# Performance work log

Measured on AMD Instinct MI355X. Metric: run time of the kernel, lower is better.

## Reference

```python
import jax, jax.numpy as jnp
import numpy as np

NEG_INF = -1e9


def setup_inputs() -> dict:
    key = jax.random.key(0)
    ks = jax.random.split(key, 6)
    B, S, D, H, Dh = 2, 2048, 1024, 16, 64
    scale = 1.0 / np.sqrt(D)
    return {
        "x": jax.random.normal(ks[0], (B, S, D), jnp.float32),
        "W_Q": jax.random.normal(ks[1], (H, D, Dh), jnp.float32) * scale,
        "b_Q": jnp.zeros((H, Dh), jnp.float32),
        "W_K": jax.random.normal(ks[2], (H, D, Dh), jnp.float32) * scale,
        "b_K": jnp.zeros((H, Dh), jnp.float32),
        "W_V": jax.random.normal(ks[3], (H, D, Dh), jnp.float32) * scale,
        "W_O": jax.random.normal(ks[4], (H, Dh, D), jnp.float32) * scale,
        "b_V": jnp.zeros((H, Dh), jnp.float32),
        "b_O": jnp.zeros((H, D), jnp.float32),
    }


def reference(x, W_Q, b_Q, W_K, b_K, W_V, W_O, b_V, b_O):
    # x: [b, s, m]; W_{Q,K,V}: [h, m, d]; W_O: [h, d, m]
    S = x.shape[1]
    d_head = W_Q.shape[-1]

    q = jnp.einsum("bqm,hmd->bqhd", x, W_Q) + b_Q  # [b, q, h, d]
    k = jnp.einsum("bkm,hmd->bkhd", x, W_K) + b_K
    v = jnp.einsum("bkm,hmd->bkhd", x, W_V) + b_V

    scores = jnp.einsum("bqhd,bkhd->bhqk", q, k) / jnp.sqrt(
        jnp.asarray(d_head, x.dtype)
    )  # [b, h, q, k] -- full score matrix, as in the unfused original
    causal = jnp.tril(jnp.ones((S, S), bool))
    scores = jnp.where(causal, scores, jnp.asarray(NEG_INF, x.dtype))
    attn = jax.nn.softmax(scores, axis=-1)

    z = jnp.einsum("bhqk,bkhd->bqhd", attn, v)  # [b, q, h, d]
    # per-head output proj then sum over heads; b_O is [h, m] per the annotation
    out = jnp.einsum("bqhd,hdm->bqm", z, W_O) + jnp.sum(b_O, axis=0)
    return out
```

## Files before the change

### kernel.cpp

```cpp
#include <hip/hip_runtime.h>
#include <cstdint>

typedef unsigned short u16;
typedef short s8v __attribute__((ext_vector_type(8)));
typedef float f4v __attribute__((ext_vector_type(4)));

__device__ __forceinline__ u16 f2b(float f) {
  uint32_t u = __float_as_uint(f);
  u = (u + 0x7FFFu + ((u >> 16) & 1u)) >> 16;
  return (u16)u;
}

__device__ __forceinline__ uint32_t pk2(float a, float b) {
  uint32_t r;
  asm("v_cvt_pk_bf16_f32 %0, %1, %2" : "=v"(r) : "v"(a), "v"(b));
  return r;
}

__device__ __forceinline__ void gload16(const u16* g, u16* l) {
  __builtin_amdgcn_global_load_lds(
      (const __attribute__((address_space(1))) void*)g,
      (__attribute__((address_space(3))) void*)l, 16, 0, 0);
}


__global__ void conv_x(const float* __restrict__ x, u16* __restrict__ xb) {
  int i = blockIdx.x * blockDim.x + threadIdx.x;
  float4 v = ((const float4*)x)[i];
  uint2 o;
  o.x = (uint32_t)f2b(v.x) | ((uint32_t)f2b(v.y) << 16);
  o.y = (uint32_t)f2b(v.z) | ((uint32_t)f2b(v.w) << 16);
  ((uint2*)xb)[i] = o;
}

__global__ void convT_w(const float* __restrict__ W, u16* __restrict__ dst) {
  __shared__ u16 tile[64][65];
  const int m0 = blockIdx.x * 64;
  const int h  = blockIdx.y;
  const int c  = threadIdx.x & 63;
  const int r4 = threadIdx.x >> 6;
  const float* Wh = W + (size_t)h * 65536;
  for (int i = 0; i < 16; ++i) {
    int lm = i * 4 + r4;
    tile[lm][c] = f2b(Wh[(size_t)(m0 + lm) * 64 + c]);
  }
  __syncthreads();
  for (int i = 0; i < 16; ++i) {
    int dd = i * 4 + r4;
    dst[((size_t)h * 64 + dd) * 1024 + m0 + c] = tile[c][dd];
  }
}

__global__ void convT_wo(const float* __restrict__ W, u16* __restrict__ dst) {
  __shared__ u16 tile[64][65];
  const int k0 = blockIdx.x * 64;
  const int m0 = blockIdx.y * 64;
  const int c  = threadIdx.x & 63;
  const int r4 = threadIdx.x >> 6;
  for (int i = 0; i < 16; ++i) {
    int lk = i * 4 + r4;
    tile[lk][c] = f2b(W[(size_t)(k0 + lk) * 1024 + m0 + c]);
  }
  __syncthreads();
  for (int i = 0; i < 16; ++i) {
    int lm = i * 4 + r4;
    dst[(size_t)(m0 + lm) * 1024 + k0 + c] = tile[c][lm];
  }
}

__global__ void convT_v(const u16* __restrict__ QKV, u16* __restrict__ VT) {
  __shared__ u16 tile[64][65];
  const int r0 = blockIdx.x * 64;
  const int c0 = blockIdx.y * 64;
  const int c  = threadIdx.x & 63;
  const int r4 = threadIdx.x >> 6;
  for (int i = 0; i < 16; ++i) {
    int lr = i * 4 + r4;
    tile[lr][c] = QKV[(size_t)(r0 + lr) * 3072 + 2048 + c0 + c];
  }
  __syncthreads();
  for (int i = 0; i < 16; ++i) {
    int lc = i * 4 + r4;
    VT[(size_t)(c0 + lc) * 4096 + r0 + c] = tile[c][lc];
  }
}

__global__ void conv_bias(const float* __restrict__ bQ, const float* __restrict__ bK,
                          const float* __restrict__ bV, const float* __restrict__ bO,
                          float* __restrict__ bqkv, float* __restrict__ bsum) {
  int t = blockIdx.x * 256 + threadIdx.x;
  if (t < 1024)       bqkv[t] = bQ[t];
  else if (t < 2048)  bqkv[t] = bK[t - 1024];
  else if (t < 3072)  bqkv[t] = bV[t - 2048];
  else {
    int m = t - 3072;
    float s = 0.f;
    for (int hh = 0; hh < 16; ++hh) s += bO[hh * 1024 + m];
    bsum[m] = s;
  }
}

template<bool OUT_F32>
__global__ void gemm_bt(const u16* __restrict__ A, const u16* __restrict__ BT,
                        const float* __restrict__ bias, void* __restrict__ Cout,
                        int N, int K, int scale_cols) {
  __shared__ __align__(16) u16 sA[128 * 32];
  __shared__ __align__(16) u16 sB[128 * 32];
  const int tid  = threadIdx.x;
  const int lane = tid & 63, wave = tid >> 6;
  const int wm = wave >> 1, wn = wave & 1;
  const int lq = lane & 15, quad = lane >> 4;
  const int m0 = blockIdx.y * 128, n0 = blockIdx.x * 128;

  f4v acc[4][4] = {};

  for (int k0 = 0; k0 < K; k0 += 32) {
    __syncthreads();
    for (int i = 0; i < 2; ++i) {
      int s = tid + i * 256;
      int row = s >> 2, part = s & 3;
      gload16(A  + (size_t)(m0 + row) * K + k0 + part * 8, &sA[s * 8]);
      gload16(BT + (size_t)(n0 + row) * K + k0 + part * 8, &sB[s * 8]);
    }
    __syncthreads();
    s8v af[4], bfr[4];
    for (int i = 0; i < 4; ++i)
      af[i]  = *(const s8v*)&sA[(wm * 64 + i * 16 + lq) * 32 + quad * 8];
    for (int j = 0; j < 4; ++j)
      bfr[j] = *(const s8v*)&sB[(wn * 64 + j * 16 + lq) * 32 + quad * 8];
    for (int i = 0; i < 4; ++i)
      for (int j = 0; j < 4; ++j)
        acc[i][j] = __builtin_amdgcn_mfma_f32_16x16x32_bf16(af[i], bfr[j], acc[i][j], 0, 0, 0);
  }

  for (int i = 0; i < 4; ++i)
    for (int j = 0; j < 4; ++j) {
      int row = m0 + wm * 64 + i * 16 + quad * 4;
      int col = n0 + wn * 64 + j * 16 + lq;
      float bb = bias[col];
      float sc = (col < scale_cols) ? 0.125f : 1.0f;
      for (int r = 0; r < 4; ++r) {
        float v = (acc[i][j][r] + bb) * sc;
        if (OUT_F32) ((float*)Cout)[(size_t)(row + r) * N + col] = v;
        else         ((u16*)Cout)[(size_t)(row + r) * N + col] = f2b(v);
      }
    }
}

__global__ __launch_bounds__(64, 2) void attn_fwd(const u16* __restrict__ QKV,
                                                  const u16* __restrict__ VT,
                                                  u16* __restrict__ Z) {
  __shared__ __align__(16) u16 sP[2][2][16 * 40];
  const int lane = threadIdx.x;
  const int lq = lane & 15, quad = lane >> 4;

  const int id   = blockIdx.x;
  const int xcd  = id & 7;
  const int slot = id >> 3;
  const int g    = xcd + 8 * (slot >> 6);
  const int s    = slot & 63;
  const int u    = (s < 32) ? (63 - s) : (s - 32);
  const int h = g & 15, b = g >> 4;
  const int qA = u * 32, qB = qA + 16;
  const int nchunk = u + 1;

  const int RS = 3072;
  const u16* base = QKV + (size_t)b * 2048 * RS;
  const u16* Qb  = base + h * 64;
  const u16* Kb  = base + 1024 + h * 64;
  const u16* VTb = VT + (size_t)h * 64 * 4096 + (size_t)b * 2048;

  s8v qfA0 = *(const s8v*)&Qb[(size_t)(qA + lq) * RS + quad * 8];
  s8v qfA1 = *(const s8v*)&Qb[(size_t)(qA + lq) * RS + 32 + quad * 8];
  s8v qfB0 = *(const s8v*)&Qb[(size_t)(qB + lq) * RS + quad * 8];
  s8v qfB1 = *(const s8v*)&Qb[(size_t)(qB + lq) * RS + 32 + quad * 8];

  f4v zA[4] = {}, zB[4] = {};
  float mA = -3.0e38f, lA = 0.f, mB = -3.0e38f, lB = 0.f;

#define LOADK(kf_, c_) do {                                                  \
    const int kk0_ = (c_) * 32;                                              \
    const u16* kr0_ = &Kb[(size_t)(kk0_ + lq) * RS + quad * 8];              \
    const u16* kr1_ = &Kb[(size_t)(kk0_ + 16 + lq) * RS + quad * 8];         \
    kf_[0] = *(const s8v*)kr0_;                                              \
    kf_[1] = *(const s8v*)(kr0_ + 32);                                       \
    kf_[2] = *(const s8v*)kr1_;                                              \
    kf_[3] = *(const s8v*)(kr1_ + 32);                                       \
  } while (0)

#define LOADV(vf_, c_) do {                                                  \
    const int kk0_ = (c_) * 32;                                              \
    vf_[0] = *(const s8v*)&VTb[(size_t)(lq)      * 4096 + kk0_ + quad * 8];  \
    vf_[1] = *(const s8v*)&VTb[(size_t)(16 + lq) * 4096 + kk0_ + quad * 8];  \
    vf_[2] = *(const s8v*)&VTb[(size_t)(32 + lq) * 4096 + kk0_ + quad * 8];  \
    vf_[3] = *(const s8v*)&VTb[(size_t)(48 + lq) * 4096 + kk0_ + quad * 8];  \
  } while (0)

  auto SMW = [&](int c, int qt0, float& mrow, float& lsum, f4v (&zacc)[4],
                 u16* sPt, f4v sacc0, f4v sacc1) {
    float s0[4], s1[4];
    for (int r = 0; r < 4; ++r) { s0[r] = sacc0[r]; s1[r] = sacc1[r]; }
    if (c + 1 == nchunk) {
      const int kb = c * 32;
      for (int r = 0; r < 4; ++r) {
        if (kb + quad * 4 + r > qt0 + lq)      s0[r] = -3.0e38f;
        if (kb + 16 + quad * 4 + r > qt0 + lq) s1[r] = -3.0e38f;
      }
    }
    float lmax = fmaxf(fmaxf(fmaxf(s0[0], s0[1]), fmaxf(s0[2], s0[3])),
                       fmaxf(fmaxf(s1[0], s1[1]), fmaxf(s1[2], s1[3])));
    if (!__all(lmax <= mrow + 8.0f)) {
      float t = lmax;
      t = fmaxf(t, __shfl_xor(t, 16, 64));
      t = fmaxf(t, __shfl_xor(t, 32, 64));
      float mnew = fmaxf(mrow, t);
      float al = __expf(mrow - mnew);
      mrow = mnew;
      lsum *= al;
      float alr[4];
      for (int r = 0; r < 4; ++r) alr[r] = __shfl(al, quad * 4 + r, 16);
      for (int dc = 0; dc < 4; ++dc)
        for (int r = 0; r < 4; ++r) zacc[dc][r] *= alr[r];
    }
    float p0[4], p1[4], acc = 0.f;
    for (int r = 0; r < 4; ++r) {
      p0[r] = __expf(s0[r] - mrow);
      p1[r] = __expf(s1[r] - mrow);
      acc += p0[r] + p1[r];
    }
    lsum += acc;
    uint2 wlo, whi;
    wlo.x = pk2(p0[0], p0[1]); wlo.y = pk2(p0[2], p0[3]);
    whi.x = pk2(p1[0], p1[1]); whi.y = pk2(p1[2], p1[3]);
    u16* rowp = &sPt[lq * 40 + quad * 4];
    *(uint2*)rowp        = wlo;
    *(uint2*)(rowp + 16) = whi;
  };

  s8v kA[4], kB[4], vA[4], vB[4];
  LOADK(kA, 0);
  LOADV(vA, 0);
  if (nchunk > 1) LOADK(kB, 1);

  {
    f4v aA0 = {}, aA1 = {}, aB0 = {}, aB1 = {};
    aA0 = __builtin_amdgcn_mfma_f32_16x16x32_bf16(kA[0], qfA0, aA0, 0, 0, 0);
    aA0 = __builtin_amdgcn_mfma_f32_16x16x32_bf16(kA[1], qfA1, aA0, 0, 0, 0);
    aA1 = __builtin_amdgcn_mfma_f32_16x16x32_bf16(kA[2], qfA0, aA1, 0, 0, 0);
    aA1 = __builtin_amdgcn_mfma_f32_16x16x32_bf16(kA[3], qfA1, aA1, 0, 0, 0);
    aB0 = __builtin_amdgcn_mfma_f32_16x16x32_bf16(kA[0], qfB0, aB0, 0, 0, 0);
    aB0 = __builtin_amdgcn_mfma_f32_16x16x32_bf16(kA[1], qfB1, aB0, 0, 0, 0);
    aB1 = __builtin_amdgcn_mfma_f32_16x16x32_bf16(kA[2], qfB0, aB1, 0, 0, 0);
    aB1 = __builtin_amdgcn_mfma_f32_16x16x32_bf16(kA[3], qfB1, aB1, 0, 0, 0);
    SMW(0, qA, mA, lA, zA, sP[0][0], aA0, aA1);
    SMW(0, qB, mB, lB, zB, sP[1][0], aB0, aB1);
  }

  auto STEP = [&](int c, s8v (&kcur)[4], s8v (&knxt)[4],
                  s8v (&vpv)[4], s8v (&vnew)[4]) {
    if (c + 1 < nchunk) LOADK(knxt, c + 1);
    LOADV(vnew, c);
    f4v aA0 = {}, aA1 = {}, aB0 = {}, aB1 = {};
    aA0 = __builtin_amdgcn_mfma_f32_16x16x32_bf16(kcur[0], qfA0, aA0, 0, 0, 0);
    aA0 = __builtin_amdgcn_mfma_f32_16x16x32_bf16(kcur[1], qfA1, aA0, 0, 0, 0);
    aA1 = __builtin_amdgcn_mfma_f32_16x16x32_bf16(kcur[2], qfA0, aA1, 0, 0, 0);
    aA1 = __builtin_amdgcn_mfma_f32_16x16x32_bf16(kcur[3], qfA1, aA1, 0, 0, 0);
    aB0 = __builtin_amdgcn_mfma_f32_16x16x32_bf16(kcur[0], qfB0, aB0, 0, 0, 0);
    aB0 = __builtin_amdgcn_mfma_f32_16x16x32_bf16(kcur[1], qfB1, aB0, 0, 0, 0);
    aB1 = __builtin_amdgcn_mfma_f32_16x16x32_bf16(kcur[2], qfB0, aB1, 0, 0, 0);
    aB1 = __builtin_amdgcn_mfma_f32_16x16x32_bf16(kcur[3], qfB1, aB1, 0, 0, 0);
    s8v pfA = *(const s8v*)&sP[0][(c + 1) & 1][lq * 40 + quad * 8];
    s8v pfB = *(const s8v*)&sP[1][(c + 1) & 1][lq * 40 + quad * 8];
    for (int dc = 0; dc < 4; ++dc)
      zA[dc] = __builtin_amdgcn_mfma_f32_16x16x32_bf16(pfA, vpv[dc], zA[dc], 0, 0, 0);
    for (int dc = 0; dc < 4; ++dc)
      zB[dc] = __builtin_amdgcn_mfma_f32_16x16x32_bf16(pfB, vpv[dc], zB[dc], 0, 0, 0);
    SMW(c, qA, mA, lA, zA, sP[0][c & 1], aA0, aA1);
    SMW(c, qB, mB, lB, zB, sP[1][c & 1], aB0, aB1);
  };

  int c = 1;
  for (; c + 1 < nchunk; c += 2) {
    STEP(c,     kB, kA, vA, vB);
    STEP(c + 1, kA, kB, vB, vA);
  }
  if (c < nchunk) STEP(c, kB, kA, vA, vB);

  {
    s8v pfA = *(const s8v*)&sP[0][(nchunk - 1) & 1][lq * 40 + quad * 8];
    s8v pfB = *(const s8v*)&sP[1][(nchunk - 1) & 1][lq * 40 + quad * 8];
    if ((nchunk - 1) & 1) {
      for (int dc = 0; dc < 4; ++dc) {
        zA[dc] = __builtin_amdgcn_mfma_f32_16x16x32_bf16(pfA, vB[dc], zA[dc], 0, 0, 0);
        zB[dc] = __builtin_amdgcn_mfma_f32_16x16x32_bf16(pfB, vB[dc], zB[dc], 0, 0, 0);
      }
    } else {
      for (int dc = 0; dc < 4; ++dc) {
        zA[dc] = __builtin_amdgcn_mfma_f32_16x16x32_bf16(pfA, vA[dc], zA[dc], 0, 0, 0);
        zB[dc] = __builtin_amdgcn_mfma_f32_16x16x32_bf16(pfB, vA[dc], zB[dc], 0, 0, 0);
      }
    }
  }
#undef LOADK
#undef LOADV

  lA += __shfl_xor(lA, 16, 64); lA += __shfl_xor(lA, 32, 64);
  lB += __shfl_xor(lB, 16, 64); lB += __shfl_xor(lB, 32, 64);
  float invA[4], invB[4];
  for (int r = 0; r < 4; ++r) {
    invA[r] = 1.0f / __shfl(lA, quad * 4 + r, 16);
    invB[r] = 1.0f / __shfl(lB, quad * 4 + r, 16);
  }
  for (int dc = 0; dc < 4; ++dc)
    for (int r = 0; r < 4; ++r) {
      size_t rowA = (size_t)b * 2048 + qA + quad * 4 + r;
      size_t rowB = (size_t)b * 2048 + qB + quad * 4 + r;
      Z[rowA * 1024 + h * 64 + dc * 16 + lq] = f2b(zA[dc][r] * invA[r]);
      Z[rowB * 1024 + h * 64 + dc * 16 + lq] = f2b(zB[dc][r] * invB[r]);
    }
}

extern "C" void kernel_launch(void* const* d_in, const int* in_sizes, int n_in,
                              void* d_out, int out_size, void* d_ws, size_t ws_size,
                              hipStream_t stream) {
  const float* x  = (const float*)d_in[0];
  const float* WQ = (const float*)d_in[1];
  const float* bQ = (const float*)d_in[2];
  const float* WK = (const float*)d_in[3];
  const float* bK = (const float*)d_in[4];
  const float* WV = (const float*)d_in[5];
  const float* WO = (const float*)d_in[6];
  const float* bV = (const float*)d_in[7];
  const float* bO = (const float*)d_in[8];
  float* out = (float*)d_out;

  uint8_t* ws = (uint8_t*)d_ws;
  u16*   xb    = (u16*)(ws);
  u16*   VTv   = (u16*)(ws);
  u16*   WTqkv = (u16*)(ws + 8388608);
  u16*   WOT   = (u16*)(ws + 14680064);
  u16*   QKV   = (u16*)(ws + 16777216);
  u16*   Zb    = (u16*)(ws + 41943040);
  float* bqkv  = (float*)(ws + 50331648);
  float* bsum  = (float*)(ws + 50343936);

  conv_x<<<4096, 256, 0, stream>>>(x, xb);
  convT_w<<<dim3(16, 16), 256, 0, stream>>>(WQ, WTqkv);
  convT_w<<<dim3(16, 16), 256, 0, stream>>>(WK, WTqkv + 1024 * 1024);
  convT_w<<<dim3(16, 16), 256, 0, stream>>>(WV, WTqkv + 2048 * 1024);
  convT_wo<<<dim3(16, 16), 256, 0, stream>>>(WO, WOT);
  conv_bias<<<16, 256, 0, stream>>>(bQ, bK, bV, bO, bqkv, bsum);

  gemm_bt<false><<<dim3(24, 32), 256, 0, stream>>>(xb, WTqkv, bqkv, (void*)QKV, 3072, 1024, 1024);
  convT_v<<<dim3(64, 16), 256, 0, stream>>>(QKV, VTv);
  attn_fwd<<<dim3(2048, 1, 1), 64, 0, stream>>>(QKV, VTv, Zb);
  gemm_bt<true><<<dim3(8, 32), 256, 0, stream>>>(Zb, WOT, bsum, (void*)out, 1024, 1024, 0);
}
```

Baseline: 230.9 us.

## Widen attention key chunks to 64, restructure pipeline, and fuse prep kernels

The attention kernel now processes 64 keys per iteration instead of 32, which halves the loop trip count and the per-chunk softmax max/rescale overhead. It uses single K/V register buffers loaded after the MFMA phase, and wraps the MFMA phases in s_setprio. The six small conversion and transpose kernels are merged into one launch, dispatched by block index, to cut launch overhead. The wider chunks raise register pressure and LDS use and waste more masked work on the diagonal chunk. Dropping the K double buffering may expose load latency.

```diff
diff --git a/kernel.cpp b/kernel.cpp
--- a/kernel.cpp
+++ b/kernel.cpp
@@ -23,48 +23,69 @@
       (__attribute__((address_space(3))) void*)l, 16, 0, 0);
 }
 
-
-__global__ void conv_x(const float* __restrict__ x, u16* __restrict__ xb) {
-  int i = blockIdx.x * blockDim.x + threadIdx.x;
-  float4 v = ((const float4*)x)[i];
-  uint2 o;
-  o.x = (uint32_t)f2b(v.x) | ((uint32_t)f2b(v.y) << 16);
-  o.y = (uint32_t)f2b(v.z) | ((uint32_t)f2b(v.w) << 16);
-  ((uint2*)xb)[i] = o;
-}
-
-__global__ void convT_w(const float* __restrict__ W, u16* __restrict__ dst) {
+__global__ void prep(const float* __restrict__ x, u16* __restrict__ xb,
+                     const float* __restrict__ WQ, const float* __restrict__ WK,
+                     const float* __restrict__ WV, const float* __restrict__ WO,
+                     u16* __restrict__ WTqkv, u16* __restrict__ WOT,
+                     const float* __restrict__ bQ, const float* __restrict__ bK,
+                     const float* __restrict__ bV, const float* __restrict__ bO,
+                     float* __restrict__ bqkv, float* __restrict__ bsum) {
   __shared__ u16 tile[64][65];
-  const int m0 = blockIdx.x * 64;
-  const int h  = blockIdx.y;
-  const int c  = threadIdx.x & 63;
-  const int r4 = threadIdx.x >> 6;
-  const float* Wh = W + (size_t)h * 65536;
-  for (int i = 0; i < 16; ++i) {
-    int lm = i * 4 + r4;
-    tile[lm][c] = f2b(Wh[(size_t)(m0 + lm) * 64 + c]);
-  }
-  __syncthreads();
-  for (int i = 0; i < 16; ++i) {
-    int dd = i * 4 + r4;
-    dst[((size_t)h * 64 + dd) * 1024 + m0 + c] = tile[c][dd];
-  }
-}
-
-__global__ void convT_wo(const float* __restrict__ W, u16* __restrict__ dst) {
-  __shared__ u16 tile[64][65];
-  const int k0 = blockIdx.x * 64;
-  const int m0 = blockIdx.y * 64;
-  const int c  = threadIdx.x & 63;
-  const int r4 = threadIdx.x >> 6;
-  for (int i = 0; i < 16; ++i) {
-    int lk = i * 4 + r4;
-    tile[lk][c] = f2b(W[(size_t)(k0 + lk) * 1024 + m0 + c]);
-  }
-  __syncthreads();
-  for (int i = 0; i < 16; ++i) {
-    int lm = i * 4 + r4;
-    dst[(size_t)(m0 + lm) * 1024 + k0 + c] = tile[c][lm];
+  const int bid = blockIdx.x;
+  const int tid = threadIdx.x;
+
+  if (bid < 4096) {
+    int i = bid * 256 + tid;
+    float4 v = ((const float4*)x)[i];
+    uint2 o;
+    o.x = (uint32_t)f2b(v.x) | ((uint32_t)f2b(v.y) << 16);
+    o.y = (uint32_t)f2b(v.z) | ((uint32_t)f2b(v.w) << 16);
+    ((uint2*)xb)[i] = o;
+  } else if (bid < 4864) {
+    int sub = bid - 4096;
+    int w = sub >> 8, sub2 = sub & 255;
+    const float* W = (w == 0) ? WQ : (w == 1) ? WK : WV;
+    u16* dst = WTqkv + (size_t)w * 1024 * 1024;
+    const int m0 = (sub2 & 15) * 64;
+    const int h  = sub2 >> 4;
+    const int c  = tid & 63;
+    const int r4 = tid >> 6;
+    const float* Wh = W + (size_t)h * 65536;
+    for (int i = 0; i < 16; ++i) {
+      int lm = i * 4 + r4;
+      tile[lm][c] = f2b(Wh[(size_t)(m0 + lm) * 64 + c]);
+    }
+    __syncthreads();
+    for (int i = 0; i < 16; ++i) {
+      int dd = i * 4 + r4;
+      dst[((size_t)h * 64 + dd) * 1024 + m0 + c] = tile[c][dd];
+    }
+  } else if (bid < 5120) {
+    int sub = bid - 4864;
+    const int k0 = (sub & 15) * 64;
+    const int m0 = (sub >> 4) * 64;
+    const int c  = tid & 63;
+    const int r4 = tid >> 6;
+    for (int i = 0; i < 16; ++i) {
+      int lk = i * 4 + r4;
+      tile[lk][c] = f2b(WO[(size_t)(k0 + lk) * 1024 + m0 + c]);
+    }
+    __syncthreads();
+    for (int i = 0; i < 16; ++i) {
+      int lm = i * 4 + r4;
+      WOT[(size_t)(m0 + lm) * 1024 + k0 + c] = tile[c][lm];
+    }
+  } else {
+    int t = (bid - 5120) * 256 + tid;
+    if (t < 1024)       bqkv[t] = bQ[t];
+    else if (t < 2048)  bqkv[t] = bK[t - 1024];
+    else if (t < 3072)  bqkv[t] = bV[t - 2048];
+    else {
+      int m = t - 3072;
+      float s = 0.f;
+      for (int hh = 0; hh < 16; ++hh) s += bO[hh * 1024 + m];
+      bsum[m] = s;
+    }
   }
 }
 
@@ -82,21 +103,6 @@
   for (int i = 0; i < 16; ++i) {
     int lc = i * 4 + r4;
     VT[(size_t)(c0 + lc) * 4096 + r0 + c] = tile[c][lc];
-  }
-}
-
-__global__ void conv_bias(const float* __restrict__ bQ, const float* __restrict__ bK,
-                          const float* __restrict__ bV, const float* __restrict__ bO,
-                          float* __restrict__ bqkv, float* __restrict__ bsum) {
-  int t = blockIdx.x * 256 + threadIdx.x;
-  if (t < 1024)       bqkv[t] = bQ[t];
-  else if (t < 2048)  bqkv[t] = bK[t - 1024];
-  else if (t < 3072)  bqkv[t] = bV[t - 2048];
-  else {
-    int m = t - 3072;
-    float s = 0.f;
-    for (int hh = 0; hh < 16; ++hh) s += bO[hh * 1024 + m];
-    bsum[m] = s;
   }
 }
 
@@ -150,7 +156,7 @@
 __global__ __launch_bounds__(64, 2) void attn_fwd(const u16* __restrict__ QKV,
                                                   const u16* __restrict__ VT,
                                                   u16* __restrict__ Z) {
-  __shared__ __align__(16) u16 sP[2][2][16 * 40];
+  __shared__ __align__(16) u16 sP[2][2][16 * 72];
   const int lane = threadIdx.x;
   const int lq = lane & 15, quad = lane >> 4;
 
@@ -162,7 +168,7 @@
   const int u    = (s < 32) ? (63 - s) : (s - 32);
   const int h = g & 15, b = g >> 4;
   const int qA = u * 32, qB = qA + 16;
-  const int nchunk = u + 1;
+  const int nchunk = u / 2 + 1;
 
   const int RS = 3072;
   const u16* base = QKV + (size_t)b * 2048 * RS;
@@ -178,37 +184,42 @@
   f4v zA[4] = {}, zB[4] = {};
   float mA = -3.0e38f, lA = 0.f, mB = -3.0e38f, lB = 0.f;
 
-#define LOADK(kf_, c_) do {                                                  \
-    const int kk0_ = (c_) * 32;                                              \
-    const u16* kr0_ = &Kb[(size_t)(kk0_ + lq) * RS + quad * 8];              \
-    const u16* kr1_ = &Kb[(size_t)(kk0_ + 16 + lq) * RS + quad * 8];         \
-    kf_[0] = *(const s8v*)kr0_;                                              \
-    kf_[1] = *(const s8v*)(kr0_ + 32);                                       \
-    kf_[2] = *(const s8v*)kr1_;                                              \
-    kf_[3] = *(const s8v*)(kr1_ + 32);                                       \
+  s8v kf[8], vf[8];
+
+#define LOADK(c_) do {                                                        \
+    const int kk0_ = (c_) * 64;                                               \
+    _Pragma("unroll")                                                         \
+    for (int i_ = 0; i_ < 4; ++i_) {                                          \
+      const u16* kr_ = &Kb[(size_t)(kk0_ + 16 * i_ + lq) * RS + quad * 8];    \
+      kf[2 * i_]     = *(const s8v*)kr_;                                      \
+      kf[2 * i_ + 1] = *(const s8v*)(kr_ + 32);                               \
+    }                                                                         \
   } while (0)
 
-#define LOADV(vf_, c_) do {                                                  \
-    const int kk0_ = (c_) * 32;                                              \
-    vf_[0] = *(const s8v*)&VTb[(size_t)(lq)      * 4096 + kk0_ + quad * 8];  \
-    vf_[1] = *(const s8v*)&VTb[(size_t)(16 + lq) * 4096 + kk0_ + quad * 8];  \
-    vf_[2] = *(const s8v*)&VTb[(size_t)(32 + lq) * 4096 + kk0_ + quad * 8];  \
-    vf_[3] = *(const s8v*)&VTb[(size_t)(48 + lq) * 4096 + kk0_ + quad * 8];  \
+#define LOADV(c_) do {                                                        \
+    const int kk0_ = (c_) * 64;                                               \
+    _Pragma("unroll")                                                         \
+    for (int d_ = 0; d_ < 4; ++d_) {                                          \
+      const u16* vr_ = &VTb[(size_t)(d_ * 16 + lq) * 4096 + kk0_ + quad * 8]; \
+      vf[d_]     = *(const s8v*)vr_;                                          \
+      vf[d_ + 4] = *(const s8v*)(vr_ + 32);                                   \
+    }                                                                         \
   } while (0)
 
   auto SMW = [&](int c, int qt0, float& mrow, float& lsum, f4v (&zacc)[4],
-                 u16* sPt, f4v sacc0, f4v sacc1) {
-    float s0[4], s1[4];
-    for (int r = 0; r < 4; ++r) { s0[r] = sacc0[r]; s1[r] = sacc1[r]; }
+                 u16* sPt, f4v (&sc)[4]) {
+    float sv[4][4];
+    for (int i = 0; i < 4; ++i)
+      for (int r = 0; r < 4; ++r) sv[i][r] = sc[i][r];
     if (c + 1 == nchunk) {
-      const int kb = c * 32;
-      for (int r = 0; r < 4; ++r) {
-        if (kb + quad * 4 + r > qt0 + lq)      s0[r] = -3.0e38f;
-        if (kb + 16 + quad * 4 + r > qt0 + lq) s1[r] = -3.0e38f;
-      }
-    }
-    float lmax = fmaxf(fmaxf(fmaxf(s0[0], s0[1]), fmaxf(s0[2], s0[3])),
-                       fmaxf(fmaxf(s1[0], s1[1]), fmaxf(s1[2], s1[3])));
+      const int kb = c * 64;
+      for (int i = 0; i < 4; ++i)
+        for (int r = 0; r < 4; ++r)
+          if (kb + 16 * i + quad * 4 + r > qt0 + lq) sv[i][r] = -3.0e38f;
+    }
+    float lmax = sv[0][0];
+    for (int i = 0; i < 4; ++i)
+      for (int r = 0; r < 4; ++r) lmax = fmaxf(lmax, sv[i][r]);
     if (!__all(lmax <= mrow + 8.0f)) {
       float t = lmax;
       t = fmaxf(t, __shfl_xor(t, 16, 64));
@@ -222,85 +233,79 @@
       for (int dc = 0; dc < 4; ++dc)
         for (int r = 0; r < 4; ++r) zacc[dc][r] *= alr[r];
     }
-    float p0[4], p1[4], acc = 0.f;
-    for (int r = 0; r < 4; ++r) {
-      p0[r] = __expf(s0[r] - mrow);
-      p1[r] = __expf(s1[r] - mrow);
-      acc += p0[r] + p1[r];
-    }
+    float acc = 0.f;
+    float p[4][4];
+    for (int i = 0; i < 4; ++i)
+      for (int r = 0; r < 4; ++r) {
+        p[i][r] = __expf(sv[i][r] - mrow);
+        acc += p[i][r];
+      }
     lsum += acc;
-    uint2 wlo, whi;
-    wlo.x = pk2(p0[0], p0[1]); wlo.y = pk2(p0[2], p0[3]);
-    whi.x = pk2(p1[0], p1[1]); whi.y = pk2(p1[2], p1[3]);
-    u16* rowp = &sPt[lq * 40 + quad * 4];
-    *(uint2*)rowp        = wlo;
-    *(uint2*)(rowp + 16) = whi;
+    for (int i = 0; i < 4; ++i) {
+      uint2 w;
+      w.x = pk2(p[i][0], p[i][1]);
+      w.y = pk2(p[i][2], p[i][3]);
+      *(uint2*)&sPt[lq * 72 + 16 * i + quad * 4] = w;
+    }
   };
 
-  s8v kA[4], kB[4], vA[4], vB[4];
-  LOADK(kA, 0);
-  LOADV(vA, 0);
-  if (nchunk > 1) LOADK(kB, 1);
-
+#define QK(aA_, aB_) do {                                                     \
+    _Pragma("unroll")                                                         \
+    for (int i_ = 0; i_ < 4; ++i_) {                                          \
+      aA_[i_] = __builtin_amdgcn_mfma_f32_16x16x32_bf16(kf[2*i_],   qfA0, aA_[i_], 0, 0, 0); \
+      aA_[i_] = __builtin_amdgcn_mfma_f32_16x16x32_bf16(kf[2*i_+1], qfA1, aA_[i_], 0, 0, 0); \
+      aB_[i_] = __builtin_amdgcn_mfma_f32_16x16x32_bf16(kf[2*i_],   qfB0, aB_[i_], 0, 0, 0); \
+      aB_[i_] = __builtin_amdgcn_mfma_f32_16x16x32_bf16(kf[2*i_+1], qfB1, aB_[i_], 0, 0, 0); \
+    }                                                                         \
+  } while (0)
+
+  auto PV = [&](int pb) {
+    s8v pA0 = *(const s8v*)&sP[0][pb][lq * 72 + quad * 8];
+    s8v pA1 = *(const s8v*)&sP[0][pb][lq * 72 + 32 + quad * 8];
+    s8v pB0 = *(const s8v*)&sP[1][pb][lq * 72 + quad * 8];
+    s8v pB1 = *(const s8v*)&sP[1][pb][lq * 72 + 32 + quad * 8];
+#pragma unroll
+    for (int d_ = 0; d_ < 4; ++d_) {
+      zA[d_] = __builtin_amdgcn_mfma_f32_16x16x32_bf16(pA0, vf[d_],     zA[d_], 0, 0, 0);
+      zA[d_] = __builtin_amdgcn_mfma_f32_16x16x32_bf16(pA1, vf[d_ + 4], zA[d_], 0, 0, 0);
+      zB[d_] = __builtin_amdgcn_mfma_f32_16x16x32_bf16(pB0, vf[d_],     zB[d_], 0, 0, 0);
+      zB[d_] = __builtin_amdgcn_mfma_f32_16x16x32_bf16(pB1, vf[d_ + 4], zB[d_], 0, 0, 0);
+    }
+  };
+
+  LOADK(0);
   {
-    f4v aA0 = {}, aA1 = {}, aB0 = {}, aB1 = {};
-    aA0 = __builtin_amdgcn_mfma_f32_16x16x32_bf16(kA[0], qfA0, aA0, 0, 0, 0);
-    aA0 = __builtin_amdgcn_mfma_f32_16x16x32_bf16(kA[1], qfA1, aA0, 0, 0, 0);
-    aA1 = __builtin_amdgcn_mfma_f32_16x16x32_bf16(kA[2], qfA0, aA1, 0, 0, 0);
-    aA1 = __builtin_amdgcn_mfma_f32_16x16x32_bf16(kA[3], qfA1, aA1, 0, 0, 0);
-    aB0 = __builtin_amdgcn_mfma_f32_16x16x32_bf16(kA[0], qfB0, aB0, 0, 0, 0);
-    aB0 = __builtin_amdgcn_mfma_f32_16x16x32_bf16(kA[1], qfB1, aB0, 0, 0, 0);
-    aB1 = __builtin_amdgcn_mfma_f32_16x16x32_bf16(kA[2], qfB0, aB1, 0, 0, 0);
-    aB1 = __builtin_amdgcn_mfma_f32_16x16x32_bf16(kA[3], qfB1, aB1, 0, 0, 0);
-    SMW(0, qA, mA, lA, zA, sP[0][0], aA0, aA1);
-    SMW(0, qB, mB, lB, zB, sP[1][0], aB0, aB1);
-  }
-
-  auto STEP = [&](int c, s8v (&kcur)[4], s8v (&knxt)[4],
-                  s8v (&vpv)[4], s8v (&vnew)[4]) {
-    if (c + 1 < nchunk) LOADK(knxt, c + 1);
-    LOADV(vnew, c);
-    f4v aA0 = {}, aA1 = {}, aB0 = {}, aB1 = {};
-    aA0 = __builtin_amdgcn_mfma_f32_16x16x32_bf16(kcur[0], qfA0, aA0, 0, 0, 0);
-    aA0 = __builtin_amdgcn_mfma_f32_16x16x32_bf16(kcur[1], qfA1, aA0, 0, 0, 0);
-    aA1 = __builtin_amdgcn_mfma_f32_16x16x32_bf16(kcur[2], qfA0, aA1, 0, 0, 0);
-    aA1 = __builtin_amdgcn_mfma_f32_16x16x32_bf16(kcur[3], qfA1, aA1, 0, 0, 0);
-    aB0 = __builtin_amdgcn_mfma_f32_16x16x32_bf16(kcur[0], qfB0, aB0, 0, 0, 0);
-    aB0 = __builtin_amdgcn_mfma_f32_16x16x32_bf16(kcur[1], qfB1, aB0, 0, 0, 0);
-    aB1 = __builtin_amdgcn_mfma_f32_16x16x32_bf16(kcur[2], qfB0, aB1, 0, 0, 0);
-    aB1 = __builtin_amdgcn_mfma_f32_16x16x32_bf16(kcur[3], qfB1, aB1, 0, 0, 0);
-    s8v pfA = *(const s8v*)&sP[0][(c + 1) & 1][lq * 40 + quad * 8];
-    s8v pfB = *(const s8v*)&sP[1][(c + 1) & 1][lq * 40 + quad * 8];
-    for (int dc = 0; dc < 4; ++dc)
-      zA[dc] = __builtin_amdgcn_mfma_f32_16x16x32_bf16(pfA, vpv[dc], zA[dc], 0, 0, 0);
-    for (int dc = 0; dc < 4; ++dc)
-      zB[dc] = __builtin_amdgcn_mfma_f32_16x16x32_bf16(pfB, vpv[dc], zB[dc], 0, 0, 0);
-    SMW(c, qA, mA, lA, zA, sP[0][c & 1], aA0, aA1);
-    SMW(c, qB, mB, lB, zB, sP[1][c & 1], aB0, aB1);
-  };
-
-  int c = 1;
-  for (; c + 1 < nchunk; c += 2) {
-    STEP(c,     kB, kA, vA, vB);
-    STEP(c + 1, kA, kB, vB, vA);
-  }
-  if (c < nchunk) STEP(c, kB, kA, vA, vB);
+    f4v aA[4] = {}, aB[4] = {};
+    __builtin_amdgcn_s_setprio(1);
+    QK(aA, aB);
+    __builtin_amdgcn_s_setprio(0);
+    if (nchunk > 1) LOADK(1);
+    LOADV(0);
+    SMW(0, qA, mA, lA, zA, sP[0][0], aA);
+    SMW(0, qB, mB, lB, zB, sP[1][0], aB);
+    asm volatile("" ::: "memory");
+  }
+
+  for (int c = 1; c < nchunk; ++c) {
+    f4v aA[4] = {}, aB[4] = {};
+    __builtin_amdgcn_s_setprio(1);
+    QK(aA, aB);
+    PV((c + 1) & 1);
+    __builtin_amdgcn_s_setprio(0);
+    asm volatile("" ::: "memory");
+    if (c + 1 < nchunk) LOADK(c + 1);
+    LOADV(c);
+    SMW(c, qA, mA, lA, zA, sP[0][c & 1], aA);
+    SMW(c, qB, mB, lB, zB, sP[1][c & 1], aB);
+    asm volatile("" ::: "memory");
+  }
 
   {
-    s8v pfA = *(const s8v*)&sP[0][(nchunk - 1) & 1][lq * 40 + quad * 8];
-    s8v pfB = *(const s8v*)&sP[1][(nchunk - 1) & 1][lq * 40 + quad * 8];
-    if ((nchunk - 1) & 1) {
-      for (int dc = 0; dc < 4; ++dc) {
-        zA[dc] = __builtin_amdgcn_mfma_f32_16x16x32_bf16(pfA, vB[dc], zA[dc], 0, 0, 0);
-        zB[dc] = __builtin_amdgcn_mfma_f32_16x16x32_bf16(pfB, vB[dc], zB[dc], 0, 0, 0);
-      }
-    } else {
-      for (int dc = 0; dc < 4; ++dc) {
-        zA[dc] = __builtin_amdgcn_mfma_f32_16x16x32_bf16(pfA, vA[dc], zA[dc], 0, 0, 0);
-        zB[dc] = __builtin_amdgcn_mfma_f32_16x16x32_bf16(pfB, vA[dc], zB[dc], 0, 0, 0);
-      }
-    }
-  }
+    __builtin_amdgcn_s_setprio(1);
+    PV((nchunk - 1) & 1);
+    __builtin_amdgcn_s_setprio(0);
+  }
+#undef QK
 #undef LOADK
 #undef LOADV
 
@@ -344,13 +349,8 @@
   float* bqkv  = (float*)(ws + 50331648);
   float* bsum  = (float*)(ws + 50343936);
 
-  conv_x<<<4096, 256, 0, stream>>>(x, xb);
-  convT_w<<<dim3(16, 16), 256, 0, stream>>>(WQ, WTqkv);
-  convT_w<<<dim3(16, 16), 256, 0, stream>>>(WK, WTqkv + 1024 * 1024);
-  convT_w<<<dim3(16, 16), 256, 0, stream>>>(WV, WTqkv + 2048 * 1024);
-  convT_wo<<<dim3(16, 16), 256, 0, stream>>>(WO, WOT);
-  conv_bias<<<16, 256, 0, stream>>>(bQ, bK, bV, bO, bqkv, bsum);
-
+  prep<<<5136, 256, 0, stream>>>(x, xb, WQ, WK, WV, WO, WTqkv, WOT,
+                                 bQ, bK, bV, bO, bqkv, bsum);
   gemm_bt<false><<<dim3(24, 32), 256, 0, stream>>>(xb, WTqkv, bqkv, (void*)QKV, 3072, 1024, 1024);
   convT_v<<<dim3(64, 16), 256, 0, stream>>>(QKV, VTv);
   attn_fwd<<<dim3(2048, 1, 1), 64, 0, stream>>>(QKV, VTv, Zb);
```

Measured after the change: 223.1 us. 3.4% less time.
